# Optimization experiments

Measured on AMD Instinct MI355X. Metric: run time of the kernel, lower is better.

Reference implementation:

```python
import jax, jax.numpy as jnp
import numpy as np

B, N, NUM_CLASS = 32, 4096, 40


def setup_inputs() -> dict:
    key = jax.random.key(0)
    ks = jax.random.split(key, 16)
    def w(k, o, i):
        return (jax.random.normal(k, (o, i), jnp.float32) / np.float32(np.sqrt(i)))
    inp = {"x": jax.random.uniform(ks[0], (B, N, 3), jnp.float32)}
    dims = [("sa1", 3, [64, 64, 128]), ("sa2", 3 + 128, [128, 128, 256]), ("sa3", 3 + 256, [256, 512, 1024])]
    ki = 1
    for name, cin, hs in dims:
        c = cin
        for j, h in enumerate(hs):
            inp[f"{name}_w{j}"] = w(jax.random.fold_in(ks[ki], j), h, c)
            inp[f"{name}_b{j}"] = jnp.zeros((h,), jnp.float32)
            c = h
        ki += 1
    for name, o, i in [("fc1", 512, 1024), ("fc2", 256, 512), ("fc3", NUM_CLASS, 256)]:
        inp[f"{name}_w"] = w(ks[ki], o, i)
        inp[f"{name}_b"] = jnp.zeros((o,), jnp.float32)
        ki += 1
    return inp


def _fps(xyz, npoint):
    # farthest point sampling for a single cloud, xyz: [N, 3] -> [npoint] indices
    n = xyz.shape[0]
    def body(carry, _):
        mind, last = carry
        d = jnp.sum((xyz - xyz[last]) ** 2, axis=-1)
        mind = jnp.minimum(mind, d)
        return (mind, jnp.argmax(mind).astype(jnp.int32)), last
    init = (jnp.full((n,), 1e10, xyz.dtype), jnp.int32(0))
    _, idx = jax.lax.scan(body, init, None, length=npoint)
    return idx


def _ball_query(new_xyz, xyz, radius, nsample):
    # new_xyz: [B,S,3], xyz: [B,N,3] -> [B,S,nsample] neighbor indices
    n = xyz.shape[1]
    sqd = (jnp.sum(new_xyz ** 2, -1)[:, :, None]
           + jnp.sum(xyz ** 2, -1)[:, None, :]
           - 2.0 * jnp.einsum('bsc,bnc->bsn', new_xyz, xyz))  # [B,S,N]
    gid = jnp.where(sqd <= radius ** 2, jnp.arange(n, dtype=jnp.int32), jnp.int32(n))
    gid = jnp.sort(gid, axis=-1)[..., :nsample]
    first = gid[..., :1]
    return jnp.where(gid == n, first, gid)


def _gather(x, idx):
    # x: [B,N,C], idx: [B,S,K] -> [B,S,K,C]
    return jax.vmap(lambda xb, ib: xb[ib])(x, idx)


def _shared_mlp(feat, layers):
    # feat: [..., C_in]; layers: list of (W [C_out,C_in], b [C_out]); 1x1 conv + ReLU (BN folded)
    for W, b in layers:
        feat = jax.nn.relu(jnp.einsum('bskc,oc->bsko', feat, W) + b)
    return feat


def _set_abstraction(xyz, feat, npoint, radius, nsample, layers):
    fidx = jax.vmap(lambda p: _fps(p, npoint))(xyz)            # [B,S]
    new_xyz = jax.vmap(lambda p, i: p[i])(xyz, fidx)           # [B,S,3]
    idx = _ball_query(new_xyz, xyz, radius, nsample)           # [B,S,K]
    gxyz = _gather(xyz, idx) - new_xyz[:, :, None, :]          # relative coords
    g = gxyz if feat is None else jnp.concatenate([gxyz, _gather(feat, idx)], axis=-1)
    g = _shared_mlp(g, layers)
    return new_xyz, jnp.max(g, axis=2)                         # max-pool over ball


def _sa_group_all(xyz, feat, layers):
    g = jnp.concatenate([xyz, feat], axis=-1)[:, None]         # [B,1,N,3+C]
    g = _shared_mlp(g, layers)
    return jnp.max(g, axis=2)[:, 0]                            # [B, 1024]


def reference(x,
              sa1_w0, sa1_b0, sa1_w1, sa1_b1, sa1_w2, sa1_b2,
              sa2_w0, sa2_b0, sa2_w1, sa2_b1, sa2_w2, sa2_b2,
              sa3_w0, sa3_b0, sa3_w1, sa3_b1, sa3_w2, sa3_b2,
              fc1_w, fc1_b, fc2_w, fc2_b, fc3_w, fc3_b):
    xyz, feat = x, None
    xyz, feat = _set_abstraction(xyz, feat, 512, 0.2, 32,
                                 [(sa1_w0, sa1_b0), (sa1_w1, sa1_b1), (sa1_w2, sa1_b2)])
    xyz, feat = _set_abstraction(xyz, feat, 128, 0.4, 64,
                                 [(sa2_w0, sa2_b0), (sa2_w1, sa2_b1), (sa2_w2, sa2_b2)])
    feat = _sa_group_all(xyz, feat,
                         [(sa3_w0, sa3_b0), (sa3_w1, sa3_b1), (sa3_w2, sa3_b2)])
    h = jax.nn.relu(feat @ fc1_w.T + fc1_b)
    h = jax.nn.relu(h @ fc2_w.T + fc2_b)
    logits = h @ fc3_w.T + fc3_b
    return jax.nn.softmax(logits, axis=-1)  # eval-mode output
```

## Files before the change

### kernel.cpp

```cpp
#include <hip/hip_runtime.h>
#include <math.h>

#define B_ 32
#define N_ 4096

typedef __attribute__((ext_vector_type(8))) short short8;
typedef __attribute__((ext_vector_type(4))) float f32x4;
typedef __attribute__((ext_vector_type(2))) float v2f;
typedef __attribute__((ext_vector_type(2))) unsigned long long u64x2;

__device__ __forceinline__ unsigned short f2bf(float f) {
    unsigned u = __float_as_uint(f);
    unsigned r = 0x7FFFu + ((u >> 16) & 1u);
    return (unsigned short)((u + r) >> 16);
}
__device__ __forceinline__ float bf2f(unsigned short h) {
    return __uint_as_float(((unsigned)h) << 16);
}
__device__ __forceinline__ void f2bfpair(float v, short& h, short& l) {
    unsigned short hh = f2bf(v);
    h = (short)hh;
    l = (short)f2bf(v - bf2f(hh));
}

#define KEY_BIAS 0x3F800000u

__device__ __forceinline__ unsigned long long u64max(unsigned long long a,
                                                     unsigned long long b) {
    return a > b ? a : b;
}
template<int CTRL>
__device__ __forceinline__ unsigned long long dpp_u64(unsigned long long k) {
    int lo = __builtin_amdgcn_mov_dpp((int)(unsigned)k, CTRL, 0xf, 0xf, true);
    int hi = __builtin_amdgcn_mov_dpp((int)(unsigned)(k >> 32), CTRL, 0xf, 0xf, true);
    return ((unsigned long long)(unsigned)hi << 32) | (unsigned)lo;
}
template<int CTRL>
__device__ __forceinline__ double dpp_dbl(double k) {
    unsigned long long u = (unsigned long long)__double_as_longlong(k);
    int lo = __builtin_amdgcn_mov_dpp((int)(unsigned)u, CTRL, 0xf, 0xf, true);
    int hi = __builtin_amdgcn_mov_dpp((int)(unsigned)(u >> 32), CTRL, 0xf, 0xf, true);
    unsigned long long r = ((unsigned long long)(unsigned)hi << 32) | (unsigned)lo;
    return __longlong_as_double((long long)r);
}
__device__ __forceinline__ unsigned long long wave_argmax_u64_leader(unsigned long long key) {
    key = u64max(key, dpp_u64<0x128>(key));
    key = u64max(key, dpp_u64<0x124>(key));
    key = u64max(key, dpp_u64<0x122>(key));
    key = u64max(key, dpp_u64<0x121>(key));
    key = u64max(key, dpp_u64<0x142>(key));
    key = u64max(key, dpp_u64<0x143>(key));
    return key;
}
__device__ __forceinline__ double wave_argmax_dbl_leader(double key) {
    key = fmax(key, dpp_dbl<0x128>(key));
    key = fmax(key, dpp_dbl<0x124>(key));
    key = fmax(key, dpp_dbl<0x122>(key));
    key = fmax(key, dpp_dbl<0x121>(key));
    key = fmax(key, dpp_dbl<0x142>(key));
    key = fmax(key, dpp_dbl<0x143>(key));
    return key;
}

struct WDesc { const float* src; short* dh; short* dl; int R, C, Cp, blk0, perm; };
struct WDescs { WDesc d[8]; float* gfeat; int gblk0, gtotal; };

__device__ __forceinline__ void wprep_body(const WDescs& W, int blk, int tid) {
    if (blk >= W.gblk0) {
        const int i = (blk - W.gblk0) * 256 + tid;
        if (i < W.gtotal) W.gfeat[i] = 0.f;
        return;
    }
    int di = 0;
#pragma unroll
    for (int k = 1; k < 8; k++) di = (blk >= W.d[k].blk0) ? k : di;
    const WDesc D = W.d[di];
    const int i = (blk - D.blk0) * 256 + tid;
    if (i >= D.R * D.Cp) return;
    const int r = i / D.Cp, c = i % D.Cp;
    int cs;
    if (D.perm) cs = (c < 128) ? c + 3 : (c < 131 ? c - 128 : -1);
    else        cs = (c < D.C) ? c : -1;
    float v = (cs >= 0) ? D.src[r * D.C + cs] : 0.f;
    short h, l;
    f2bfpair(v, h, l);
    D.dh[i] = h; D.dl[i] = l;
}

template<int N, int NPOINT, int NT, int FPSB>
__global__ __launch_bounds__(NT, 1) void fps_wprep_kernel(
    const float* __restrict__ xyz, float* __restrict__ outXyz, WDescs W) {
#pragma clang fp contract(off)
    const int t = threadIdx.x;
    if (blockIdx.x >= FPSB) {
        wprep_body(W, blockIdx.x - FPSB, t);
        return;
    }
    const int b = blockIdx.x;
    constexpr int PPT = N / NT;
    constexpr int PP2 = PPT / 2;
    constexpr int NW = (NT + 63) / 64;
    __shared__ float ps[N][4];
    __shared__ __align__(16) double red[2][NW];
    __shared__ float outBuf[NPOINT * 3];
    const float* base = xyz + (size_t)b * N * 3;
    for (int j = t; j < N; j += NT) {
        ps[j][0] = base[j * 3 + 0];
        ps[j][1] = base[j * 3 + 1];
        ps[j][2] = base[j * 3 + 2];
    }
    __syncthreads();
    v2f px2[PP2], py2[PP2], pz2[PP2], mn2[PP2];
    unsigned nA[PP2], nB[PP2];
#pragma unroll
    for (int j = 0; j < PP2; j++) {
        const int p0 = t + (2 * j) * NT;
        const int p1 = t + (2 * j + 1) * NT;
        f32x4 a = *(const f32x4*)&ps[p0][0];
        f32x4 c = *(const f32x4*)&ps[p1][0];
        px2[j] = (v2f){a[0], c[0]};
        py2[j] = (v2f){a[1], c[1]};
        pz2[j] = (v2f){a[2], c[2]};
        mn2[j] = (v2f){1e10f, 1e10f};
        nA[j] = ~(unsigned)p0;
        nB[j] = ~(unsigned)p1;
    }
#pragma unroll
    for (int j = 0; j < PP2; j++)
        asm volatile("" : "+v"(px2[j]), "+v"(py2[j]), "+v"(pz2[j]));
    float lx = ps[0][0], ly = ps[0][1], lz = ps[0][2];
    if (t == 0) {
        outBuf[0] = lx; outBuf[1] = ly; outBuf[2] = lz;
    }
    for (int it = 1; it < NPOINT; it++) {
        const v2f lx2 = (v2f){lx, lx};
        const v2f ly2 = (v2f){ly, ly};
        const v2f lz2 = (v2f){lz, lz};
        double k0 = 0.0, k1 = 0.0, k2 = 0.0, k3 = 0.0;
#pragma unroll
        for (int j = 0; j < PP2; j++) {
            v2f dx = px2[j] - lx2;
            v2f dy = py2[j] - ly2;
            v2f dz = pz2[j] - lz2;
            v2f t0 = dx * dx, t1 = dy * dy, t2 = dz * dz;
            v2f d2 = (t0 + t1) + t2;
            float m0 = fminf(mn2[j][0], d2[0]);
            float m1 = fminf(mn2[j][1], d2[1]);
            mn2[j][0] = m0;
            mn2[j][1] = m1;
            double da = __longlong_as_double((long long)(
                ((unsigned long long)(__float_as_uint(m0) + KEY_BIAS) << 32) | nA[j]));
            double db = __longlong_as_double((long long)(
                ((unsigned long long)(__float_as_uint(m1) + KEY_BIAS) << 32) | nB[j]));
            if (j & 1) { k2 = fmax(k2, da); k3 = fmax(k3, db); }
            else       { k0 = fmax(k0, da); k1 = fmax(k1, db); }
        }
        double key = fmax(fmax(k0, k1), fmax(k2, k3));
        key = wave_argmax_dbl_leader(key);
        const int par = it & 1;
        if ((t & 63) == 63) red[par][t >> 6] = key;
        __syncthreads();
        u64x2 r01 = *(const u64x2*)&red[par][0];
        u64x2 r23 = *(const u64x2*)&red[par][2];
        double b0 = __longlong_as_double((long long)r01[0]);
        double b1 = __longlong_as_double((long long)r01[1]);
        double b2 = __longlong_as_double((long long)r23[0]);
        double b3 = __longlong_as_double((long long)r23[1]);
        double best = fmax(fmax(b0, b1), fmax(b2, b3));
        const int fi = (int)(~(unsigned)(unsigned long long)__double_as_longlong(best));
        f32x4 c4 = *(const f32x4*)&ps[fi][0];
        lx = c4[0]; ly = c4[1]; lz = c4[2];
        if (t == 0) {
            outBuf[it * 3 + 0] = lx;
            outBuf[it * 3 + 1] = ly;
            outBuf[it * 3 + 2] = lz;
        }
    }
    __syncthreads();
    float* dst = outXyz + (size_t)b * NPOINT * 3;
    for (int j = t; j < NPOINT * 3; j += NT) dst[j] = outBuf[j];
}

template<int N, int NS>
__device__ __forceinline__ void ballquery_body(
    const float* __restrict__ xyz, const float* __restrict__ newXyz,
    int* __restrict__ outIdx, int S, float r2, int qid, int lane) {
#pragma clang fp contract(off)
    const int b = qid / S;
    const float* q = newXyz + (size_t)qid * 3;
    const float qx = q[0], qy = q[1], qz = q[2];
    const float qn = (qx * qx + qy * qy) + qz * qz;
    const float* base = xyz + (size_t)b * N * 3;
    int* dst = outIdx + (size_t)qid * NS;
    int cnt = 0, first = 0;
    for (int p0 = 0; p0 < N; p0 += 64) {
        const int p = p0 + lane;
        const float x = base[p * 3 + 0];
        const float y = base[p * 3 + 1];
        const float z = base[p * 3 + 2];
        const float pn = (x * x + y * y) + z * z;
        const float dot = (qx * x + qy * y) + qz * z;
        const float sqd = (qn + pn) - 2.0f * dot;
        const unsigned long long mask = __ballot(sqd <= r2);
        if (mask) {
            if (cnt == 0) first = p0 + __ffsll((unsigned long long)mask) - 1;
            const int prefix = __builtin_amdgcn_mbcnt_hi(
                (unsigned)(mask >> 32),
                __builtin_amdgcn_mbcnt_lo((unsigned)mask, 0));
            const bool in = (mask >> lane) & 1ull;
            const int pos = cnt + prefix;
            if (in && pos < NS) dst[pos] = p;
            cnt += __popcll(mask);
            if (cnt >= NS) break;
        }
    }
    for (int i = cnt + lane; i < NS; i += 64) dst[i] = first;
}

template<int BQB, int NQ, int NS, int SQ, int NF, int NPF>
__global__ __launch_bounds__(256) void bq_fps_kernel(
    const float* __restrict__ xyzQ, const float* __restrict__ newXyzQ,
    int* __restrict__ outIdxQ, float r2,
    const float* __restrict__ xyzF, float* __restrict__ outXyzF) {
#pragma clang fp contract(off)
    const int t = threadIdx.x;
    const int lane = t & 63, wv = t >> 6;
    __shared__ float ps[NF][4];
    if (blockIdx.x < BQB) {
        ballquery_body<NQ, NS>(xyzQ, newXyzQ, outIdxQ, SQ, r2,
                               blockIdx.x * 4 + wv, lane);
        return;
    }
    const int b = blockIdx.x - BQB;
    const float* base = xyzF + (size_t)b * NF * 3;
    for (int j = t; j < NF; j += 256) {
        ps[j][0] = base[j * 3 + 0];
        ps[j][1] = base[j * 3 + 1];
        ps[j][2] = base[j * 3 + 2];
    }
    __syncthreads();
    if (t >= 64) return;
    constexpr int PPT = NF / 64;
    float px[PPT], py[PPT], pz[PPT], mind[PPT];
    unsigned notp[PPT];
#pragma unroll
    for (int i = 0; i < PPT; i++) {
        int p = t + i * 64;
        f32x4 c4 = *(const f32x4*)&ps[p][0];
        px[i] = c4[0]; py[i] = c4[1]; pz[i] = c4[2];
        mind[i] = 1e10f;
        notp[i] = ~(unsigned)p;
    }
    float lx = ps[0][0], ly = ps[0][1], lz = ps[0][2];
    if (t == 0) {
        outXyzF[(size_t)b * NPF * 3 + 0] = lx;
        outXyzF[(size_t)b * NPF * 3 + 1] = ly;
        outXyzF[(size_t)b * NPF * 3 + 2] = lz;
    }
    for (int it = 1; it < NPF; it++) {
        unsigned long long key = 0;
#pragma unroll
        for (int i = 0; i < PPT; i++) {
            float dx = px[i] - lx, dy = py[i] - ly, dz = pz[i] - lz;
            float t0 = dx * dx, t1 = dy * dy, t2 = dz * dz;
            float d = (t0 + t1) + t2;
            float m = fminf(mind[i], d);
            mind[i] = m;
            unsigned long long k =
                ((unsigned long long)__float_as_uint(m) << 32) | notp[i];
            key = u64max(key, k);
        }
        key = wave_argmax_u64_leader(key);
        const int lo = __shfl((int)(unsigned)key, 63);
        const int fi = (int)(~(unsigned)lo);
        f32x4 c4 = *(const f32x4*)&ps[fi][0];
        lx = c4[0]; ly = c4[1]; lz = c4[2];
        if (t == 0) {
            outXyzF[((size_t)b * NPF + it) * 3 + 0] = lx;
            outXyzF[((size_t)b * NPF + it) * 3 + 1] = ly;
            outXyzF[((size_t)b * NPF + it) * 3 + 2] = lz;
        }
    }
}

template<int NT, int KS>
__device__ __forceinline__ void mfma_layer(
    const short* Aph, const short* Apl, const int sA,
    const short* __restrict__ Wph, const short* __restrict__ Wpl, const int sW,
    f32x4* acc, const int n0, const int mh, const int lr, const int lq) {
#pragma unroll
    for (int ks = 0; ks < KS; ks++) {
        const int ka = ks * 32 + lq * 8;
        short8 a_h[2], a_l[2];
#pragma unroll
        for (int mt = 0; mt < 2; mt++) {
            const int m = (mh * 2 + mt) * 16 + lr;
            a_h[mt] = *(const short8*)(Aph + m * sA + ka);
            a_l[mt] = *(const short8*)(Apl + m * sA + ka);
        }
#pragma unroll
        for (int nt = 0; nt < NT; nt++) {
            const int n = n0 + nt * 16 + lr;
            short8 b_h = *(const short8*)(Wph + (size_t)n * sW + ka);
            short8 b_l = *(const short8*)(Wpl + (size_t)n * sW + ka);
#pragma unroll
            for (int mt = 0; mt < 2; mt++) {
                f32x4 c = acc[mt * NT + nt];
                c = __builtin_amdgcn_mfma_f32_16x16x32_bf16(a_h[mt], b_h, c, 0, 0, 0);
                c = __builtin_amdgcn_mfma_f32_16x16x32_bf16(a_h[mt], b_l, c, 0, 0, 0);
                c = __builtin_amdgcn_mfma_f32_16x16x32_bf16(a_l[mt], b_h, c, 0, 0, 0);
                acc[mt * NT + nt] = c;
            }
        }
    }
}

template<int NT>
__device__ __forceinline__ void init_bias(f32x4* acc, const float* __restrict__ bias,
                                          const int n0, const int lr) {
#pragma unroll
    for (int nt = 0; nt < NT; nt++) {
        float bv = bias[n0 + nt * 16 + lr];
        f32x4 c = {bv, bv, bv, bv};
        acc[0 * NT + nt] = c;
        acc[1 * NT + nt] = c;
    }
}

template<int NT>
__device__ __forceinline__ void store_split(
    const f32x4* acc, short* Hp, short* Lp, const int stride,
    const int n0, const int mh, const int lr, const int lq) {
#pragma unroll
    for (int mt = 0; mt < 2; mt++)
#pragma unroll
        for (int nt = 0; nt < NT; nt++)
#pragma unroll
            for (int r = 0; r < 4; r++) {
                float v = fmaxf(acc[mt * NT + nt][r], 0.f);
                short h, l;
                f2bfpair(v, h, l);
                const int m = (mh * 2 + mt) * 16 + lq * 4 + r;
                const int n = n0 + nt * 16 + lr;
                Hp[m * stride + n] = h;
                Lp[m * stride + n] = l;
            }
}

#define T1 72
template<int SAB>
__global__ __launch_bounds__(256) void sa1_bq2_kernel(
    const float* __restrict__ x, const float* __restrict__ nxyz1,
    const int* __restrict__ idx,
    const float* __restrict__ w0, const float* __restrict__ b0,
    const short* __restrict__ w1h, const short* __restrict__ w1l,
    const float* __restrict__ b1,
    const short* __restrict__ w2h, const short* __restrict__ w2l,
    const float* __restrict__ b2,
    short* __restrict__ feat1h, short* __restrict__ feat1l,
    const float* __restrict__ nxyz2, int* __restrict__ idx2, float r2q) {
    const int t = threadIdx.x;
    const int lane = t & 63, wv = t >> 6;
    if (blockIdx.x >= SAB) {
        ballquery_body<512, 64>(nxyz1, nxyz2, idx2, 128, r2q,
                                (blockIdx.x - SAB) * 4 + wv, lane);
        return;
    }
    const int g0 = blockIdx.x * 2;
    const int b = g0 >> 9;
    const int lr = lane & 15, lq = lane >> 4;
    const int mh = wv & 1, nh = wv >> 1;
    __shared__ float gx[64][4];
    __shared__ short H1h[64 * T1], H1l[64 * T1];
    __shared__ short H2h[64 * T1], H2l[64 * T1];
    if (t < 64) {
        int g = g0 + (t >> 5);
        int id = idx[(size_t)g * 32 + (t & 31)];
        const float* pp = x + ((size_t)b * N_ + id) * 3;
        const float* cc = nxyz1 + (size_t)g * 3;
        gx[t][0] = pp[0] - cc[0];
        gx[t][1] = pp[1] - cc[1];
        gx[t][2] = pp[2] - cc[2];
    }
    __syncthreads();
    {
        const int m = t >> 2, oc = (t & 3) * 16;
        float a0 = gx[m][0], a1 = gx[m][1], a2 = gx[m][2];
        short8 hv0, hv1, lv0, lv1;
#pragma unroll
        for (int i = 0; i < 16; i++) {
            int o = oc + i;
            float v = fmaf(w0[o * 3 + 0], a0,
                      fmaf(w0[o * 3 + 1], a1,
                      fmaf(w0[o * 3 + 2], a2, b0[o])));
            v = fmaxf(v, 0.f);
            short h, l;
            f2bfpair(v, h, l);
            if (i < 8) { hv0[i] = h; lv0[i] = l; }
            else       { hv1[i - 8] = h; lv1[i - 8] = l; }
        }
        *(short8*)&H1h[m * T1 + oc]     = hv0;
        *(short8*)&H1h[m * T1 + oc + 8] = hv1;
        *(short8*)&H1l[m * T1 + oc]     = lv0;
        *(short8*)&H1l[m * T1 + oc + 8] = lv1;
    }
    __syncthreads();
    {
        f32x4 acc[4];
        init_bias<2>(acc, b1, nh * 32, lr);
        mfma_layer<2, 2>(H1h, H1l, T1, w1h, w1l, 64, acc, nh * 32, mh, lr, lq);
        store_split<2>(acc, H2h, H2l, T1, nh * 32, mh, lr, lq);
    }
    __syncthreads();
    {
        f32x4 acc[8];
        init_bias<4>(acc, b2, nh * 64, lr);
        mfma_layer<4, 2>(H2h, H2l, T1, w2h, w2l, 64, acc, nh * 64, mh, lr, lq);
#pragma unroll
        for (int nt = 0; nt < 4; nt++) {
            float v = 0.f;
#pragma unroll
            for (int mt = 0; mt < 2; mt++)
#pragma unroll
                for (int r = 0; r < 4; r++)
                    v = fmaxf(v, acc[mt * 4 + nt][r]);
            v = fmaxf(v, __shfl_xor(v, 16));
            v = fmaxf(v, __shfl_xor(v, 32));
            if (lane < 16) {
                short h, l;
                f2bfpair(v, h, l);
                size_t o = (size_t)(g0 + mh) * 128 + nh * 64 + nt * 16 + lane;
                feat1h[o] = h;
                feat1l[o] = l;
            }
        }
    }
}

#define S1 168
#define S2 136
__global__ __launch_bounds__(256) void sa2_mfma_kernel(
    const float* __restrict__ xyz1,
    const short* __restrict__ feat1h, const short* __restrict__ feat1l,
    const float* __restrict__ newXyz, const int* __restrict__ idx,
    const short* __restrict__ w0h, const short* __restrict__ w0l,
    const float* __restrict__ b0,
    const short* __restrict__ w1h, const short* __restrict__ w1l,
    const float* __restrict__ b1,
    const short* __restrict__ w2h, const short* __restrict__ w2l,
    const float* __restrict__ b2,
    short* __restrict__ a3h, short* __restrict__ a3l) {
    const int g = blockIdx.x;
    const int b = g >> 7;
    const int t = threadIdx.x;
    const int lane = t & 63, wv = t >> 6;
    const int lr = lane & 15, lq = lane >> 4;
    const int mh = wv & 1, nh = wv >> 1;
    __shared__ short Ah[64 * S1], Al[64 * S1];
    __shared__ short Hh[64 * S2], Hl[64 * S2];
    __shared__ float pmax[2][256];
    __shared__ int ids[64];
    if (t < 64) ids[t] = idx[(size_t)g * 64 + t];
    __syncthreads();
    {
        const int m = t >> 2, q = t & 3;
        const int id = ids[m];
        const size_t frow = ((size_t)b * 512 + id) * 128;
#pragma unroll
        for (int c8 = 0; c8 < 4; c8++) {
            const int k = q * 32 + c8 * 8;
            *(short8*)&Ah[m * S1 + k] = *(const short8*)(feat1h + frow + k);
            *(short8*)&Al[m * S1 + k] = *(const short8*)(feat1l + frow + k);
        }
        if (t < 64) {
            const int id2 = ids[t];
            short8 zz = {0, 0, 0, 0, 0, 0, 0, 0};
            *(short8*)&Ah[t * S1 + 128] = zz;
            *(short8*)&Ah[t * S1 + 136] = zz;
            *(short8*)&Ah[t * S1 + 144] = zz;
            *(short8*)&Ah[t * S1 + 152] = zz;
            *(short8*)&Al[t * S1 + 128] = zz;
            *(short8*)&Al[t * S1 + 136] = zz;
            *(short8*)&Al[t * S1 + 144] = zz;
            *(short8*)&Al[t * S1 + 152] = zz;
            const float* prow = xyz1 + ((size_t)b * 512 + id2) * 3;
            const float* crow = newXyz + (size_t)g * 3;
#pragma unroll
            for (int c = 0; c < 3; c++) {
                short h, l;
                f2bfpair(prow[c] - crow[c], h, l);
                Ah[t * S1 + 128 + c] = h;
                Al[t * S1 + 128 + c] = l;
            }
        }
    }
    __syncthreads();
    {
        f32x4 acc[8];
        init_bias<4>(acc, b0, nh * 64, lr);
        mfma_layer<4, 5>(Ah, Al, S1, w0h, w0l, 160, acc, nh * 64, mh, lr, lq);
        store_split<4>(acc, Hh, Hl, S2, nh * 64, mh, lr, lq);
    }
    __syncthreads();
    {
        f32x4 acc[8];
        init_bias<4>(acc, b1, nh * 64, lr);
        mfma_layer<4, 4>(Hh, Hl, S2, w1h, w1l, 128, acc, nh * 64, mh, lr, lq);
        store_split<4>(acc, Ah, Al, S2, nh * 64, mh, lr, lq);
    }
    __syncthreads();
    {
        f32x4 acc[16];
        init_bias<8>(acc, b2, nh * 128, lr);
        mfma_layer<8, 4>(Ah, Al, S2, w2h, w2l, 128, acc, nh * 128, mh, lr, lq);
#pragma unroll
        for (int nt = 0; nt < 8; nt++) {
            float v = 0.f;
#pragma unroll
            for (int mt = 0; mt < 2; mt++)
#pragma unroll
                for (int r = 0; r < 4; r++)
                    v = fmaxf(v, acc[mt * 8 + nt][r]);
            v = fmaxf(v, __shfl_xor(v, 16));
            v = fmaxf(v, __shfl_xor(v, 32));
            if (lane < 16) pmax[mh][nh * 128 + nt * 16 + lane] = v;
        }
    }
    __syncthreads();
    {
        float v = fmaxf(pmax[0][t], pmax[1][t]);
        short h, l;
        f2bfpair(v, h, l);
        a3h[(size_t)g * 288 + 3 + t] = h;
        a3l[(size_t)g * 288 + 3 + t] = l;
        if (t < 3) {
            f2bfpair(newXyz[(size_t)g * 3 + t], h, l);
            a3h[(size_t)g * 288 + t] = h;
            a3l[(size_t)g * 288 + t] = l;
        }
        if (t >= 227) {
            a3h[(size_t)g * 288 + t + 32] = 0;
            a3l[(size_t)g * 288 + t + 32] = 0;
        }
    }
}

template<int OUT_MODE>
__global__ __launch_bounds__(256) void mfma_gemm_kernel(
    const short* __restrict__ Agh, const short* __restrict__ Agl, const int Kp,
    const short* __restrict__ Wh, const short* __restrict__ Wl,
    const float* __restrict__ bias,
    float* __restrict__ outF, short* __restrict__ outH,
    short* __restrict__ outL, const int N) {
    const int t = threadIdx.x;
    const int lane = t & 63, wv = t >> 6;
    const int lr = lane & 15, lq = lane >> 4;
    const int mh = wv & 1, nh = wv >> 1;
    const int m0 = blockIdx.y * 64;
    const int n0 = blockIdx.x * 128 + nh * 64;
    __shared__ short Ah[64 * 40], Al[64 * 40];
    f32x4 acc[8];
#pragma unroll
    for (int nt = 0; nt < 4; nt++) {
        float bv = bias[n0 + nt * 16 + lr];
        f32x4 c = {bv, bv, bv, bv};
        acc[nt] = c; acc[4 + nt] = c;
    }
    const int srow = t >> 2, sk = (t & 3) * 8;
    for (int kt = 0; kt < Kp; kt += 32) {
        {
            const size_t src = (size_t)(m0 + srow) * Kp + kt + sk;
            *(short8*)&Ah[srow * 40 + sk] = *(const short8*)(Agh + src);
            *(short8*)&Al[srow * 40 + sk] = *(const short8*)(Agl + src);
        }
        __syncthreads();
        short8 a_h[2], a_l[2];
#pragma unroll
        for (int mt = 0; mt < 2; mt++) {
            const int m = mh * 32 + mt * 16 + lr;
            a_h[mt] = *(const short8*)&Ah[m * 40 + lq * 8];
            a_l[mt] = *(const short8*)&Al[m * 40 + lq * 8];
        }
#pragma unroll
        for (int nt = 0; nt < 4; nt++) {
            const int n = n0 + nt * 16 + lr;
            short8 b_h = *(const short8*)(Wh + (size_t)n * Kp + kt + lq * 8);
            short8 b_l = *(const short8*)(Wl + (size_t)n * Kp + kt + lq * 8);
#pragma unroll
            for (int mt = 0; mt < 2; mt++) {
                f32x4 c = acc[mt * 4 + nt];
                c = __builtin_amdgcn_mfma_f32_16x16x32_bf16(a_h[mt], b_h, c, 0, 0, 0);
                c = __builtin_amdgcn_mfma_f32_16x16x32_bf16(a_h[mt], b_l, c, 0, 0, 0);
                c = __builtin_amdgcn_mfma_f32_16x16x32_bf16(a_l[mt], b_h, c, 0, 0, 0);
                acc[mt * 4 + nt] = c;
            }
        }
        __syncthreads();
    }
    if (OUT_MODE == 2) {
        const int batch = blockIdx.y >> 1;
#pragma unroll
        for (int nt = 0; nt < 4; nt++) {
            float v = 0.f;
#pragma unroll
            for (int mt = 0; mt < 2; mt++)
#pragma unroll
                for (int r = 0; r < 4; r++)
                    v = fmaxf(v, acc[mt * 4 + nt][r]);
            v = fmaxf(v, __shfl_xor(v, 16));
            v = fmaxf(v, __shfl_xor(v, 32));
            if (lane < 16)
                atomicMax((int*)&outF[(size_t)batch * N + n0 + nt * 16 + lane],
                          __float_as_int(v));
        }
        return;
    }
#pragma unroll
    for (int mt = 0; mt < 2; mt++)
#pragma unroll
        for (int nt = 0; nt < 4; nt++)
#pragma unroll
            for (int r = 0; r < 4; r++) {
                const int m = m0 + mh * 32 + mt * 16 + lq * 4 + r;
                const int n = n0 + nt * 16 + lr;
                float v = fmaxf(acc[mt * 4 + nt][r], 0.f);
                short h, l;
                f2bfpair(v, h, l);
                outH[(size_t)m * N + n] = h;
                outL[(size_t)m * N + n] = l;
            }
}

template<int K, int OPW, int ACT>
__global__ __launch_bounds__(256) void fc_kernel(
    const float* __restrict__ in, const float* __restrict__ w,
    const float* __restrict__ bias, float* __restrict__ out, const int O) {
    const int batch = blockIdx.y;
    const int t = threadIdx.x, lane = t & 63, wv = t >> 6;
    __shared__ float f[K];
    for (int j = t; j < K; j += 256) f[j] = in[batch * K + j];
    __syncthreads();
    const int o0 = blockIdx.x * (4 * OPW) + wv * OPW;
#pragma unroll
    for (int i = 0; i < OPW; i++) {
        const int o = o0 + i;
        const float* wr = w + (size_t)o * K;
        float a = 0.f;
#pragma unroll
        for (int c = lane; c < K; c += 64) a = fmaf(wr[c], f[c], a);
#pragma unroll
        for (int off = 32; off > 0; off >>= 1) a += __shfl_xor(a, off);
        if (lane == 0) {
            float v = a + bias[o];
            out[batch * O + o] = ACT ? fmaxf(v, 0.f) : v;
        }
    }
}

__global__ __launch_bounds__(256) void fc3_softmax_kernel(
    const float* __restrict__ in, const float* __restrict__ w3,
    const float* __restrict__ b3, float* __restrict__ out) {
    const int b = blockIdx.x, t = threadIdx.x, lane = t & 63, wv = t >> 6;
    __shared__ float f[256];
    __shared__ float lg[40];
    f[t] = in[b * 256 + t];
    __syncthreads();
#pragma unroll
    for (int i = 0; i < 10; i++) {
        const int o = wv * 10 + i;
        const float* wr = w3 + (size_t)o * 256;
        float a = 0.f;
#pragma unroll
        for (int c = lane; c < 256; c += 64) a = fmaf(wr[c], f[c], a);
#pragma unroll
        for (int off = 32; off > 0; off >>= 1) a += __shfl_xor(a, off);
        if (lane == 0) lg[o] = a + b3[o];
    }
    __syncthreads();
    if (t < 64) {
        float v = (t < 40) ? lg[t] : -INFINITY;
        float m = v;
#pragma unroll
        for (int off = 32; off > 0; off >>= 1) m = fmaxf(m, __shfl_xor(m, off));
        float e = (t < 40) ? expf(v - m) : 0.f;
        float s = e;
#pragma unroll
        for (int off = 32; off > 0; off >>= 1) s += __shfl_xor(s, off);
        if (t < 40) out[b * 40 + t] = e / s;
    }
}

extern "C" void kernel_launch(void* const* d_in, const int* in_sizes, int n_in,
                              void* d_out, int out_size, void* d_ws, size_t ws_size,
                              hipStream_t stream) {
    (void)in_sizes; (void)n_in; (void)out_size; (void)ws_size;
    const float* x      = (const float*)d_in[0];
    const float* sa1w0  = (const float*)d_in[1];
    const float* sa1b0  = (const float*)d_in[2];
    const float* sa1w1  = (const float*)d_in[3];
    const float* sa1b1  = (const float*)d_in[4];
    const float* sa1w2  = (const float*)d_in[5];
    const float* sa1b2  = (const float*)d_in[6];
    const float* sa2w0  = (const float*)d_in[7];
    const float* sa2b0  = (const float*)d_in[8];
    const float* sa2w1  = (const float*)d_in[9];
    const float* sa2b1  = (const float*)d_in[10];
    const float* sa2w2  = (const float*)d_in[11];
    const float* sa2b2  = (const float*)d_in[12];
    const float* sa3w0  = (const float*)d_in[13];
    const float* sa3b0  = (const float*)d_in[14];
    const float* sa3w1  = (const float*)d_in[15];
    const float* sa3b1  = (const float*)d_in[16];
    const float* sa3w2  = (const float*)d_in[17];
    const float* sa3b2  = (const float*)d_in[18];
    const float* fc1w   = (const float*)d_in[19];
    const float* fc1b   = (const float*)d_in[20];
    const float* fc2w   = (const float*)d_in[21];
    const float* fc2b   = (const float*)d_in[22];
    const float* fc3w   = (const float*)d_in[23];
    const float* fc3b   = (const float*)d_in[24];
    float* outp = (float*)d_out;

    char* ws = (char*)d_ws;
    size_t off = 0;
    auto alloc = [&](size_t bytes) {
        void* p = ws + off;
        off += (bytes + 255) & ~(size_t)255;
        return p;
    };
    float* nxyz1   = (float*)alloc((size_t)B_ * 512 * 3 * 4);
    int*   idx1    = (int*)  alloc((size_t)B_ * 512 * 32 * 4);
    short* feat1h  = (short*)alloc((size_t)B_ * 512 * 128 * 2);
    short* feat1l  = (short*)alloc((size_t)B_ * 512 * 128 * 2);
    float* nxyz2   = (float*)alloc((size_t)B_ * 128 * 3 * 4);
    int*   idx2    = (int*)  alloc((size_t)B_ * 128 * 64 * 4);
    short* a3h     = (short*)alloc((size_t)4096 * 288 * 2);
    short* a3l     = (short*)alloc((size_t)4096 * 288 * 2);
    short* h3ah    = (short*)alloc((size_t)4096 * 256 * 2);
    short* h3al    = (short*)alloc((size_t)4096 * 256 * 2);
    short* h3bh    = (short*)alloc((size_t)4096 * 512 * 2);
    short* h3bl    = (short*)alloc((size_t)4096 * 512 * 2);
    float* gfeat   = (float*)alloc((size_t)B_ * 1024 * 4);
    float* h1      = (float*)alloc((size_t)B_ * 512 * 4);
    float* h2      = (float*)alloc((size_t)B_ * 256 * 4);
    short* w1h_s1 = (short*)alloc((size_t)64 * 64 * 2);
    short* w1l_s1 = (short*)alloc((size_t)64 * 64 * 2);
    short* w2h_s1 = (short*)alloc((size_t)128 * 64 * 2);
    short* w2l_s1 = (short*)alloc((size_t)128 * 64 * 2);
    short* w0h_s2 = (short*)alloc((size_t)128 * 160 * 2);
    short* w0l_s2 = (short*)alloc((size_t)128 * 160 * 2);
    short* w1h_s2 = (short*)alloc((size_t)128 * 128 * 2);
    short* w1l_s2 = (short*)alloc((size_t)128 * 128 * 2);
    short* w2h_s2 = (short*)alloc((size_t)256 * 128 * 2);
    short* w2l_s2 = (short*)alloc((size_t)256 * 128 * 2);
    short* w0h_s3 = (short*)alloc((size_t)256 * 288 * 2);
    short* w0l_s3 = (short*)alloc((size_t)256 * 288 * 2);
    short* w1h_s3 = (short*)alloc((size_t)512 * 256 * 2);
    short* w1l_s3 = (short*)alloc((size_t)512 * 256 * 2);
    short* w2h_s3 = (short*)alloc((size_t)1024 * 512 * 2);
    short* w2l_s3 = (short*)alloc((size_t)1024 * 512 * 2);

    {
        WDescs W;
        const float* srcs[8] = {sa1w1, sa1w2, sa2w0, sa2w1, sa2w2, sa3w0, sa3w1, sa3w2};
        short* dhs[8] = {w1h_s1, w2h_s1, w0h_s2, w1h_s2, w2h_s2, w0h_s3, w1h_s3, w2h_s3};
        short* dls[8] = {w1l_s1, w2l_s1, w0l_s2, w1l_s2, w2l_s2, w0l_s3, w1l_s3, w2l_s3};
        int Rs[8]  = {64, 128, 128, 128, 256, 256, 512, 1024};
        int Cs[8]  = {64, 64, 131, 128, 128, 259, 256, 512};
        int Cps[8] = {64, 64, 160, 128, 128, 288, 256, 512};
        int blk = 0;
        for (int k = 0; k < 8; k++) {
            W.d[k] = {srcs[k], dhs[k], dls[k], Rs[k], Cs[k], Cps[k], blk,
                      (k == 2) ? 1 : 0};
            blk += (Rs[k] * Cps[k] + 255) / 256;
        }
        W.gfeat = gfeat;
        W.gblk0 = blk;
        W.gtotal = B_ * 1024;
        blk += (B_ * 1024 + 255) / 256;
        fps_wprep_kernel<4096, 512, 256, B_><<<B_ + blk, 256, 0, stream>>>(
            x, nxyz1, W);
    }

    bq_fps_kernel<4096, 4096, 32, 512, 512, 128>
        <<<4096 + B_, 256, 0, stream>>>(
            x, nxyz1, idx1, 0.04f, nxyz1, nxyz2);
    sa1_bq2_kernel<8192><<<8192 + 1024, 256, 0, stream>>>(
        x, nxyz1, idx1, sa1w0, sa1b0,
        w1h_s1, w1l_s1, sa1b1, w2h_s1, w2l_s1, sa1b2, feat1h, feat1l,
        nxyz2, idx2, 0.16f);
    sa2_mfma_kernel<<<B_ * 128, 256, 0, stream>>>(
        nxyz1, feat1h, feat1l, nxyz2, idx2,
        w0h_s2, w0l_s2, sa2b0, w1h_s2, w1l_s2, sa2b1, w2h_s2, w2l_s2, sa2b2,
        a3h, a3l);
    mfma_gemm_kernel<1><<<dim3(2, 64), 256, 0, stream>>>(
        a3h, a3l, 288, w0h_s3, w0l_s3, sa3b0, nullptr, h3ah, h3al, 256);
    mfma_gemm_kernel<1><<<dim3(4, 64), 256, 0, stream>>>(
        h3ah, h3al, 256, w1h_s3, w1l_s3, sa3b1, nullptr, h3bh, h3bl, 512);
    mfma_gemm_kernel<2><<<dim3(8, 64), 256, 0, stream>>>(
        h3bh, h3bl, 512, w2h_s3, w2l_s3, sa3b2, gfeat, nullptr, nullptr, 1024);
    fc_kernel<1024, 16, 1><<<dim3(8, B_), 256, 0, stream>>>(
        gfeat, fc1w, fc1b, h1, 512);
    fc_kernel<512, 16, 1><<<dim3(4, B_), 256, 0, stream>>>(
        h1, fc2w, fc2b, h2, 256);
    fc3_softmax_kernel<<<B_, 256, 0, stream>>>(h2, fc3w, fc3b, outp);
}
```

Baseline: 945.5 us.

## Schedule FPS blocks first, vectorize FPS argmax, fuse FC head into one kernel

Three unrelated changes. The fused FPS and ball-query kernels now put the long serial FPS blocks (and the second ball-query blocks) at the front of the grid, so they start early and overlap with the many short blocks. The FPS inner loop is rewritten to use packed v2f arithmetic and a double-typed fmax argmax with a biased key instead of a u64 compare. The three FC layers plus softmax are merged into one kernel with one block per batch, which removes two launches but leaves only 32 blocks, each reading the full fc1 and fc2 weights.

```diff
diff --git a/kernel.cpp b/kernel.cpp
--- a/kernel.cpp
+++ b/kernel.cpp
@@ -28,12 +28,6 @@
 __device__ __forceinline__ unsigned long long u64max(unsigned long long a,
                                                      unsigned long long b) {
     return a > b ? a : b;
-}
-template<int CTRL>
-__device__ __forceinline__ unsigned long long dpp_u64(unsigned long long k) {
-    int lo = __builtin_amdgcn_mov_dpp((int)(unsigned)k, CTRL, 0xf, 0xf, true);
-    int hi = __builtin_amdgcn_mov_dpp((int)(unsigned)(k >> 32), CTRL, 0xf, 0xf, true);
-    return ((unsigned long long)(unsigned)hi << 32) | (unsigned)lo;
 }
 template<int CTRL>
 __device__ __forceinline__ double dpp_dbl(double k) {
@@ -42,15 +36,6 @@
     int hi = __builtin_amdgcn_mov_dpp((int)(unsigned)(u >> 32), CTRL, 0xf, 0xf, true);
     unsigned long long r = ((unsigned long long)(unsigned)hi << 32) | (unsigned)lo;
     return __longlong_as_double((long long)r);
-}
-__device__ __forceinline__ unsigned long long wave_argmax_u64_leader(unsigned long long key) {
-    key = u64max(key, dpp_u64<0x128>(key));
-    key = u64max(key, dpp_u64<0x124>(key));
-    key = u64max(key, dpp_u64<0x122>(key));
-    key = u64max(key, dpp_u64<0x121>(key));
-    key = u64max(key, dpp_u64<0x142>(key));
-    key = u64max(key, dpp_u64<0x143>(key));
-    return key;
 }
 __device__ __forceinline__ double wave_argmax_dbl_leader(double key) {
     key = fmax(key, dpp_dbl<0x128>(key));
@@ -217,7 +202,7 @@
     for (int i = cnt + lane; i < NS; i += 64) dst[i] = first;
 }
 
-template<int BQB, int NQ, int NS, int SQ, int NF, int NPF>
+template<int FPB, int BQB, int NQ, int NS, int SQ, int NF, int NPF>
 __global__ __launch_bounds__(256) void bq_fps_kernel(
     const float* __restrict__ xyzQ, const float* __restrict__ newXyzQ,
     int* __restrict__ outIdxQ, float r2,
@@ -226,12 +211,12 @@
     const int t = threadIdx.x;
     const int lane = t & 63, wv = t >> 6;
     __shared__ float ps[NF][4];
-    if (blockIdx.x < BQB) {
+    if (blockIdx.x >= FPB) {
         ballquery_body<NQ, NS>(xyzQ, newXyzQ, outIdxQ, SQ, r2,
-                               blockIdx.x * 4 + wv, lane);
+                               (blockIdx.x - FPB) * 4 + wv, lane);
         return;
     }
-    const int b = blockIdx.x - BQB;
+    const int b = blockIdx.x;
     const float* base = xyzF + (size_t)b * NF * 3;
     for (int j = t; j < NF; j += 256) {
         ps[j][0] = base[j * 3 + 0];
@@ -241,15 +226,21 @@
     __syncthreads();
     if (t >= 64) return;
     constexpr int PPT = NF / 64;
-    float px[PPT], py[PPT], pz[PPT], mind[PPT];
-    unsigned notp[PPT];
-#pragma unroll
-    for (int i = 0; i < PPT; i++) {
-        int p = t + i * 64;
-        f32x4 c4 = *(const f32x4*)&ps[p][0];
-        px[i] = c4[0]; py[i] = c4[1]; pz[i] = c4[2];
-        mind[i] = 1e10f;
-        notp[i] = ~(unsigned)p;
+    constexpr int PP2 = PPT / 2;
+    v2f px2[PP2], py2[PP2], pz2[PP2], mn2[PP2];
+    unsigned nA[PP2], nB[PP2];
+#pragma unroll
+    for (int j = 0; j < PP2; j++) {
+        const int p0 = t + (2 * j) * 64;
+        const int p1 = t + (2 * j + 1) * 64;
+        f32x4 a = *(const f32x4*)&ps[p0][0];
+        f32x4 c = *(const f32x4*)&ps[p1][0];
+        px2[j] = (v2f){a[0], c[0]};
+        py2[j] = (v2f){a[1], c[1]};
+        pz2[j] = (v2f){a[2], c[2]};
+        mn2[j] = (v2f){1e10f, 1e10f};
+        nA[j] = ~(unsigned)p0;
+        nB[j] = ~(unsigned)p1;
     }
     float lx = ps[0][0], ly = ps[0][1], lz = ps[0][2];
     if (t == 0) {
@@ -258,20 +249,32 @@
         outXyzF[(size_t)b * NPF * 3 + 2] = lz;
     }
     for (int it = 1; it < NPF; it++) {
-        unsigned long long key = 0;
-#pragma unroll
-        for (int i = 0; i < PPT; i++) {
-            float dx = px[i] - lx, dy = py[i] - ly, dz = pz[i] - lz;
-            float t0 = dx * dx, t1 = dy * dy, t2 = dz * dz;
-            float d = (t0 + t1) + t2;
-            float m = fminf(mind[i], d);
-            mind[i] = m;
-            unsigned long long k =
-                ((unsigned long long)__float_as_uint(m) << 32) | notp[i];
-            key = u64max(key, k);
-        }
-        key = wave_argmax_u64_leader(key);
-        const int lo = __shfl((int)(unsigned)key, 63);
+        const v2f lx2 = (v2f){lx, lx};
+        const v2f ly2 = (v2f){ly, ly};
+        const v2f lz2 = (v2f){lz, lz};
+        double k0 = 0.0, k1 = 0.0;
+#pragma unroll
+        for (int j = 0; j < PP2; j++) {
+            v2f dx = px2[j] - lx2;
+            v2f dy = py2[j] - ly2;
+            v2f dz = pz2[j] - lz2;
+            v2f t0 = dx * dx, t1 = dy * dy, t2 = dz * dz;
+            v2f d2 = (t0 + t1) + t2;
+            float m0 = fminf(mn2[j][0], d2[0]);
+            float m1 = fminf(mn2[j][1], d2[1]);
+            mn2[j][0] = m0;
+            mn2[j][1] = m1;
+            double da = __longlong_as_double((long long)(
+                ((unsigned long long)(__float_as_uint(m0) + KEY_BIAS) << 32) | nA[j]));
+            double db = __longlong_as_double((long long)(
+                ((unsigned long long)(__float_as_uint(m1) + KEY_BIAS) << 32) | nB[j]));
+            k0 = fmax(k0, da);
+            k1 = fmax(k1, db);
+        }
+        double key = fmax(k0, k1);
+        key = wave_argmax_dbl_leader(key);
+        const int lo = __shfl(
+            (int)(unsigned)(unsigned long long)__double_as_longlong(key), 63);
         const int fi = (int)(~(unsigned)lo);
         f32x4 c4 = *(const f32x4*)&ps[fi][0];
         lx = c4[0]; ly = c4[1]; lz = c4[2];
@@ -348,7 +351,7 @@
 }
 
 #define T1 72
-template<int SAB>
+template<int BQ2B>
 __global__ __launch_bounds__(256) void sa1_bq2_kernel(
     const float* __restrict__ x, const float* __restrict__ nxyz1,
     const int* __restrict__ idx,
@@ -361,12 +364,12 @@
     const float* __restrict__ nxyz2, int* __restrict__ idx2, float r2q) {
     const int t = threadIdx.x;
     const int lane = t & 63, wv = t >> 6;
-    if (blockIdx.x >= SAB) {
+    if (blockIdx.x < BQ2B) {
         ballquery_body<512, 64>(nxyz1, nxyz2, idx2, 128, r2q,
-                                (blockIdx.x - SAB) * 4 + wv, lane);
+                                blockIdx.x * 4 + wv, lane);
         return;
     }
-    const int g0 = blockIdx.x * 2;
+    const int g0 = (blockIdx.x - BQ2B) * 2;
     const int b = g0 >> 9;
     const int lr = lane & 15, lq = lane >> 4;
     const int mh = wv & 1, nh = wv >> 1;
@@ -631,39 +634,49 @@
             }
 }
 
-template<int K, int OPW, int ACT>
-__global__ __launch_bounds__(256) void fc_kernel(
-    const float* __restrict__ in, const float* __restrict__ w,
-    const float* __restrict__ bias, float* __restrict__ out, const int O) {
-    const int batch = blockIdx.y;
-    const int t = threadIdx.x, lane = t & 63, wv = t >> 6;
-    __shared__ float f[K];
-    for (int j = t; j < K; j += 256) f[j] = in[batch * K + j];
-    __syncthreads();
-    const int o0 = blockIdx.x * (4 * OPW) + wv * OPW;
-#pragma unroll
-    for (int i = 0; i < OPW; i++) {
-        const int o = o0 + i;
-        const float* wr = w + (size_t)o * K;
-        float a = 0.f;
-#pragma unroll
-        for (int c = lane; c < K; c += 64) a = fmaf(wr[c], f[c], a);
-#pragma unroll
-        for (int off = 32; off > 0; off >>= 1) a += __shfl_xor(a, off);
-        if (lane == 0) {
-            float v = a + bias[o];
-            out[batch * O + o] = ACT ? fmaxf(v, 0.f) : v;
-        }
-    }
-}
-
-__global__ __launch_bounds__(256) void fc3_softmax_kernel(
-    const float* __restrict__ in, const float* __restrict__ w3,
+__global__ __launch_bounds__(256) void fc_head_kernel(
+    const float* __restrict__ in, const float* __restrict__ w1,
+    const float* __restrict__ b1, const float* __restrict__ w2,
+    const float* __restrict__ b2, const float* __restrict__ w3,
     const float* __restrict__ b3, float* __restrict__ out) {
     const int b = blockIdx.x, t = threadIdx.x, lane = t & 63, wv = t >> 6;
-    __shared__ float f[256];
+    __shared__ float f0[1024];
+    __shared__ float f1[512];
+    __shared__ float f2[256];
     __shared__ float lg[40];
-    f[t] = in[b * 256 + t];
+    *(f32x4*)&f0[t * 4] = *(const f32x4*)&in[b * 1024 + t * 4];
+    __syncthreads();
+#pragma unroll
+    for (int ch = 0; ch < 8; ch++) {
+        const int o0 = ch * 64 + wv * 16;
+#pragma unroll
+        for (int i = 0; i < 16; i++) {
+            const int o = o0 + i;
+            const float* wr = w1 + (size_t)o * 1024;
+            float a = 0.f;
+#pragma unroll
+            for (int c = lane; c < 1024; c += 64) a = fmaf(wr[c], f0[c], a);
+#pragma unroll
+            for (int off = 32; off > 0; off >>= 1) a += __shfl_xor(a, off);
+            if (lane == 0) f1[o] = fmaxf(a + b1[o], 0.f);
+        }
+    }
+    __syncthreads();
+#pragma unroll
+    for (int ch = 0; ch < 4; ch++) {
+        const int o0 = ch * 64 + wv * 16;
+#pragma unroll
+        for (int i = 0; i < 16; i++) {
+            const int o = o0 + i;
+            const float* wr = w2 + (size_t)o * 512;
+            float a = 0.f;
+#pragma unroll
+            for (int c = lane; c < 512; c += 64) a = fmaf(wr[c], f1[c], a);
+#pragma unroll
+            for (int off = 32; off > 0; off >>= 1) a += __shfl_xor(a, off);
+            if (lane == 0) f2[o] = fmaxf(a + b2[o], 0.f);
+        }
+    }
     __syncthreads();
 #pragma unroll
     for (int i = 0; i < 10; i++) {
@@ -671,7 +684,7 @@
         const float* wr = w3 + (size_t)o * 256;
         float a = 0.f;
 #pragma unroll
-        for (int c = lane; c < 256; c += 64) a = fmaf(wr[c], f[c], a);
+        for (int c = lane; c < 256; c += 64) a = fmaf(wr[c], f2[c], a);
 #pragma unroll
         for (int off = 32; off > 0; off >>= 1) a += __shfl_xor(a, off);
         if (lane == 0) lg[o] = a + b3[o];
@@ -741,8 +754,6 @@
     short* h3bh    = (short*)alloc((size_t)4096 * 512 * 2);
     short* h3bl    = (short*)alloc((size_t)4096 * 512 * 2);
     float* gfeat   = (float*)alloc((size_t)B_ * 1024 * 4);
-    float* h1      = (float*)alloc((size_t)B_ * 512 * 4);
-    float* h2      = (float*)alloc((size_t)B_ * 256 * 4);
     short* w1h_s1 = (short*)alloc((size_t)64 * 64 * 2);
     short* w1l_s1 = (short*)alloc((size_t)64 * 64 * 2);
     short* w2h_s1 = (short*)alloc((size_t)128 * 64 * 2);
@@ -782,10 +793,10 @@
             x, nxyz1, W);
     }
 
-    bq_fps_kernel<4096, 4096, 32, 512, 512, 128>
-        <<<4096 + B_, 256, 0, stream>>>(
+    bq_fps_kernel<B_, 4096, 4096, 32, 512, 512, 128>
+        <<<B_ + 4096, 256, 0, stream>>>(
             x, nxyz1, idx1, 0.04f, nxyz1, nxyz2);
-    sa1_bq2_kernel<8192><<<8192 + 1024, 256, 0, stream>>>(
+    sa1_bq2_kernel<1024><<<1024 + 8192, 256, 0, stream>>>(
         x, nxyz1, idx1, sa1w0, sa1b0,
         w1h_s1, w1l_s1, sa1b1, w2h_s1, w2l_s1, sa1b2, feat1h, feat1l,
         nxyz2, idx2, 0.16f);
@@ -799,9 +810,6 @@
         h3ah, h3al, 256, w1h_s3, w1l_s3, sa3b1, nullptr, h3bh, h3bl, 512);
     mfma_gemm_kernel<2><<<dim3(8, 64), 256, 0, stream>>>(
         h3bh, h3bl, 512, w2h_s3, w2l_s3, sa3b2, gfeat, nullptr, nullptr, 1024);
-    fc_kernel<1024, 16, 1><<<dim3(8, B_), 256, 0, stream>>>(
-        gfeat, fc1w, fc1b, h1, 512);
-    fc_kernel<512, 16, 1><<<dim3(4, B_), 256, 0, stream>>>(
-        h1, fc2w, fc2b, h2, 256);
-    fc3_softmax_kernel<<<B_, 256, 0, stream>>>(h2, fc3w, fc3b, outp);
-}
+    fc_head_kernel<<<B_, 256, 0, stream>>>(
+        gfeat, fc1w, fc1b, fc2w, fc2b, fc3w, fc3b, outp);
+}
```

Result: slower. 1.402 ms (+48.2%).
